# Optimization experiments

Measured on AMD Instinct MI355X. Metric: run time of the kernel, lower is better.

The kernel has to match this reference:

```python
import jax, jax.numpy as jnp
import numpy as np

B = 131072   # batch rows in the (pooled) sparse tensor
C = 512      # conv_out4
J = 7        # jnt_dim
H = 512      # linear_out
TAU_MAX = 1.0  # undefined global in source; torque cap, taken as 1.0
EPS = 1e-5


def layer_norm(x, g, b):
    m = jnp.mean(x, axis=-1, keepdims=True)
    v = jnp.var(x, axis=-1, keepdims=True)
    return (x - m) * jax.lax.rsqrt(v + EPS) * g + b


def setup_inputs() -> dict:
    key = jax.random.key(0)
    ks = jax.random.split(key, 6)
    return {
        "features": jax.random.normal(ks[0], (B, C), dtype=jnp.float32),
        "coords": jax.random.randint(ks[1], (B,), 0, B),  # batch indices (col 0 of ME coords)
        "jnt_pos": jax.random.normal(ks[2], (B, J), dtype=jnp.float32),
        "jnt_goal": jax.random.normal(ks[3], (B, J), dtype=jnp.float32),
        "ln1_g": jnp.ones((C,), jnp.float32),
        "ln1_b": jnp.zeros((C,), jnp.float32),
        "W1": jax.random.normal(ks[4], (C + 2 * J, H), dtype=jnp.float32) / np.sqrt(C + 2 * J),
        "b1": jnp.zeros((H,), jnp.float32),
        "ln2_g": jnp.ones((H,), jnp.float32),
        "ln2_b": jnp.zeros((H,), jnp.float32),
        "W2": jax.random.normal(ks[5], (H, J), dtype=jnp.float32) / np.sqrt(H),
        "b2": jnp.zeros((J,), jnp.float32),
    }


def reference(features, coords, jnt_pos, jnt_goal,
              ln1_g, ln1_b, W1, b1, ln2_g, ln2_b, W2, b2):
    # to_dense_tnsr: y = zeros_like(features); for c in coords: y[c] = features[c]
    # vectorized: single gather + scatter (duplicate writes carry identical values)
    y = jnp.zeros_like(features).at[coords].set(features[coords])
    # norm = LayerNorm(512) -> SELU   (dropout in eval mode: identity)
    x = jax.nn.selu(layer_norm(y, ln1_g, ln1_b))
    # cat((jnt_pos, jnt_goal, x), dim=1)
    x = jnp.concatenate([jnt_pos, jnt_goal, x], axis=1)  # [B, 2J+C]
    # linear = Linear -> LayerNorm -> SELU
    x = jax.nn.selu(layer_norm(x @ W1 + b1, ln2_g, ln2_b))
    # out = Linear -> Tanh, scaled by tau_max
    return jnp.tanh(x @ W2 + b2) * TAU_MAX
```

## Files before the change

### kernel.cpp

```cpp
#include <hip/hip_runtime.h>

#define B_ROWS   131072
#define MTILE    64
#define KCHUNKS  17
#define LDA      552
#define LDX      528
#define W1F_OFF  ((size_t)B_ROWS)
#define W2F_OFF  (W1F_OFF + (size_t)544 * 512 * 2)

typedef _Float16 f16x8 __attribute__((ext_vector_type(8)));
typedef float    f32x4 __attribute__((ext_vector_type(4)));

__device__ inline unsigned short f2h(float f) {
  _Float16 h = (_Float16)f;
  return __builtin_bit_cast(unsigned short, h);
}
__device__ inline float selu_f(float x) {
  const float lam = 1.0507009873554805f, alp = 1.6732632423543772f;
  return x > 0.f ? lam * x : lam * alp * (__expf(x) - 1.f);
}

__global__ void scatter_mask(const int* __restrict__ coords,
                             unsigned char* __restrict__ mask) {
  int i = blockIdx.x * 256 + threadIdx.x;
  mask[coords[i]] = 1u;
}

__global__ void build_wf(const float* __restrict__ W1, const float* __restrict__ W2,
                         unsigned short* __restrict__ W1f, unsigned short* __restrict__ W2f) {
  int tid = threadIdx.x;
  if (blockIdx.x < 544) {
    int fragIdx = blockIdx.x;
    int ni = fragIdx & 3;
    int c  = (fragIdx >> 2) % 17;
    int wq = fragIdx / 68;
    int nbase = wq * 64 + ni * 16;
    __shared__ float t[32][17];
    int kl = tid >> 4, nl = tid & 15;
    int kg = c * 32 + kl;
    float v = 0.f;
    if (kg < 512)      v = W1[(size_t)(kg + 14) * 512 + nbase + nl];
    else if (kg < 526) v = W1[(size_t)(kg - 512) * 512 + nbase + nl];
    t[kl][nl] = v;
    __syncthreads();
    int lane = tid >> 3, e = tid & 7;
    int k2 = ((lane >> 4) & 3) * 8 + e;
    int n2 = lane & 15;
    W1f[(size_t)fragIdx * 512 + tid] = f2h(t[k2][n2]);
  } else {
    int c2 = blockIdx.x - 544;
    int lane = tid >> 3, e = tid & 7;
    int n = lane & 15, quad = (lane >> 4) & 3;
    int k = c2 * 32 + quad * 8 + e;
    float v = (n < 7) ? W2[(size_t)k * 7 + n] : 0.f;
    W2f[(size_t)c2 * 512 + tid] = f2h(v);
  }
}

struct __align__(16) SMem {
  char buf[70656];
  float rsum[MTILE], rsq[MTILE], mean2[MTILE], rstd2[MTILE];
};

__global__ __launch_bounds__(512, 4) void actor_main(
    const float* __restrict__ feat, const unsigned char* __restrict__ mask,
    const float* __restrict__ jp, const float* __restrict__ jg,
    const float* __restrict__ ln1g, const float* __restrict__ ln1b,
    const unsigned short* __restrict__ W1f, const float* __restrict__ b1,
    const float* __restrict__ ln2g, const float* __restrict__ ln2b,
    const unsigned short* __restrict__ W2f, const float* __restrict__ b2,
    float* __restrict__ out) {
  __shared__ SMem sm;
  unsigned short* At = (unsigned short*)sm.buf;
  unsigned short* X2 = (unsigned short*)sm.buf;
  float*          O  = (float*)(sm.buf + 64 * LDX * 2);

  const int tid  = threadIdx.x;
  const int wq   = tid >> 6;
  const int lane = tid & 63;
  const int m0   = blockIdx.x * MTILE;
  const int mrow = lane & 15;
  const int quad = lane >> 4;

  if (tid < MTILE) { sm.rsum[tid] = 0.f; sm.rsq[tid] = 0.f; }

  const unsigned short* wBase = W1f + (size_t)wq * 68 * 512 + lane * 8;
  f16x8 bE[4], bO[4];
#pragma unroll
  for (int ni = 0; ni < 4; ++ni)
    bE[ni] = *(const f16x8*)(wBase + (size_t)ni * 512);

  {
    const int arow = tid >> 3;
    const int acg  = tid & 7;
    const int row  = m0 + arow;
    const float4* frow = (const float4*)feat + (size_t)row * 128 + acg;
    float4 f[16];
    float s = 0.f, q = 0.f;
#pragma unroll
    for (int c = 0; c < 16; ++c) {
      float4 v = frow[(size_t)c * 8];
      f[c] = v;
      s += v.x + v.y + v.z + v.w;
      q += v.x * v.x + v.y * v.y + v.z * v.z + v.w * v.w;
    }
    s += __shfl_xor(s, 1); q += __shfl_xor(q, 1);
    s += __shfl_xor(s, 2); q += __shfl_xor(q, 2);
    s += __shfl_xor(s, 4); q += __shfl_xor(q, 4);
    float mk   = mask[row] ? 1.f : 0.f;
    float mean = mk * s * (1.f / 512.f);
    float msq  = mk * q * (1.f / 512.f);
    float rstd = rsqrtf(msq - mean * mean + 1e-5f);
#pragma unroll
    for (int c = 0; c < 16; ++c) {
      float4 g = ((const float4*)ln1g)[c * 8 + acg];
      float4 b = ((const float4*)ln1b)[c * 8 + acg];
      union { unsigned short us[4]; uint2 u; } pk;
      pk.us[0] = f2h(selu_f((f[c].x * mk - mean) * rstd * g.x + b.x));
      pk.us[1] = f2h(selu_f((f[c].y * mk - mean) * rstd * g.y + b.y));
      pk.us[2] = f2h(selu_f((f[c].z * mk - mean) * rstd * g.z + b.z));
      pk.us[3] = f2h(selu_f((f[c].w * mk - mean) * rstd * g.w + b.w));
      *(uint2*)&At[arow * LDA + c * 32 + acg * 4] = pk.u;
    }
    {
      union { unsigned short us[4]; uint2 u; } pk;
#pragma unroll
      for (int q2 = 0; q2 < 4; ++q2) {
        int kk = acg * 4 + q2;
        float val = 0.f;
        if (kk < 7)       val = jp[(size_t)row * 7 + kk];
        else if (kk < 14) val = jg[(size_t)row * 7 + kk - 7];
        pk.us[q2] = f2h(val);
      }
      *(uint2*)&At[arow * LDA + 512 + acg * 4] = pk.u;
    }
  }
  __syncthreads();

  f32x4 acc[4][4];
#pragma unroll
  for (int mi = 0; mi < 4; ++mi)
#pragma unroll
    for (int ni = 0; ni < 4; ++ni) acc[mi][ni] = (f32x4){0.f, 0.f, 0.f, 0.f};

  const unsigned short* aB = At + mrow * LDA + quad * 8;

  auto loadB = [&](f16x8* dst, int c) {
#pragma unroll
    for (int ni = 0; ni < 4; ++ni)
      dst[ni] = *(const f16x8*)(wBase + (size_t)(c * 4 + ni) * 512);
  };
  auto step = [&](const f16x8* bF, int c) {
    f16x8 a[4];
#pragma unroll
    for (int mi = 0; mi < 4; ++mi)
      a[mi] = *(const f16x8*)(aB + mi * 16 * LDA + c * 32);
#pragma unroll
    for (int mi = 0; mi < 4; ++mi)
#pragma unroll
      for (int ni = 0; ni < 4; ++ni)
        acc[mi][ni] = __builtin_amdgcn_mfma_f32_16x16x32_f16(a[mi], bF[ni], acc[mi][ni], 0, 0, 0);
  };

  for (int c = 0; c < KCHUNKS - 1; c += 2) {
    loadB(bO, c + 1);
    step(bE, c);
    loadB(bE, c + 2);
    step(bO, c + 1);
  }
  step(bE, 16);

  f16x8 bW2[2];
  bW2[0] = *(const f16x8*)&W2f[(size_t)(2 * wq)     * 512 + lane * 8];
  bW2[1] = *(const f16x8*)&W2f[(size_t)(2 * wq + 1) * 512 + lane * 8];

  float b1v[4], g2v[4], bl2v[4];
#pragma unroll
  for (int ni = 0; ni < 4; ++ni) {
    int col = wq * 64 + ni * 16 + mrow;
    b1v[ni] = b1[col]; g2v[ni] = ln2g[col]; bl2v[ni] = ln2b[col];
  }
#pragma unroll
  for (int mi = 0; mi < 4; ++mi)
#pragma unroll
    for (int reg = 0; reg < 4; ++reg) {
      int r = mi * 16 + quad * 4 + reg;
      float s = 0.f, q = 0.f;
#pragma unroll
      for (int ni = 0; ni < 4; ++ni) {
        float v = acc[mi][ni][reg] + b1v[ni];
        acc[mi][ni][reg] = v;
        s += v; q += v * v;
      }
      s += __shfl_xor(s, 1); q += __shfl_xor(q, 1);
      s += __shfl_xor(s, 2); q += __shfl_xor(q, 2);
      s += __shfl_xor(s, 4); q += __shfl_xor(q, 4);
      s += __shfl_xor(s, 8); q += __shfl_xor(q, 8);
      if ((lane & 15) == 0) { atomicAdd(&sm.rsum[r], s); atomicAdd(&sm.rsq[r], q); }
    }
  __syncthreads();
  if (tid < MTILE) {
    float mean = sm.rsum[tid] * (1.f / 512.f);
    float var  = sm.rsq[tid] * (1.f / 512.f) - mean * mean;
    sm.mean2[tid] = mean;
    sm.rstd2[tid] = rsqrtf(var + 1e-5f);
  }
  O[tid] = 0.f;
  __syncthreads();
#pragma unroll
  for (int mi = 0; mi < 4; ++mi)
#pragma unroll
    for (int ni = 0; ni < 4; ++ni)
#pragma unroll
      for (int reg = 0; reg < 4; ++reg) {
        int r = mi * 16 + quad * 4 + reg;
        int col = wq * 64 + ni * 16 + mrow;
        float v = (acc[mi][ni][reg] - sm.mean2[r]) * sm.rstd2[r] * g2v[ni] + bl2v[ni];
        X2[r * LDX + col] = f2h(selu_f(v));
      }
  __syncthreads();

  {
    f32x4 acc2[4];
#pragma unroll
    for (int mi = 0; mi < 4; ++mi) acc2[mi] = (f32x4){0.f, 0.f, 0.f, 0.f};
#pragma unroll
    for (int j = 0; j < 2; ++j) {
      int c2 = 2 * wq + j;
#pragma unroll
      for (int mi = 0; mi < 4; ++mi) {
        f16x8 a = *(const f16x8*)&X2[(mi * 16 + mrow) * LDX + c2 * 32 + quad * 8];
        acc2[mi] = __builtin_amdgcn_mfma_f32_16x16x32_f16(a, bW2[j], acc2[mi], 0, 0, 0);
      }
    }
#pragma unroll
    for (int mi = 0; mi < 4; ++mi)
#pragma unroll
      for (int reg = 0; reg < 4; ++reg)
        if (mrow < 7)
          atomicAdd(&O[(mi * 16 + quad * 4 + reg) * 8 + mrow], acc2[mi][reg]);
  }
  __syncthreads();
  {
    int r = tid >> 3, c = tid & 7;
    if (c < 7)
      out[(size_t)(m0 + r) * 7 + c] = tanhf(O[tid] + b2[c]);
  }
}

extern "C" void kernel_launch(void* const* d_in, const int* in_sizes, int n_in,
                              void* d_out, int out_size, void* d_ws, size_t ws_size,
                              hipStream_t stream) {
  const float* feat  = (const float*)d_in[0];
  const int*   crd   = (const int*)d_in[1];
  const float* jp    = (const float*)d_in[2];
  const float* jg    = (const float*)d_in[3];
  const float* ln1g  = (const float*)d_in[4];
  const float* ln1b  = (const float*)d_in[5];
  const float* W1    = (const float*)d_in[6];
  const float* b1    = (const float*)d_in[7];
  const float* ln2g  = (const float*)d_in[8];
  const float* ln2b  = (const float*)d_in[9];
  const float* W2    = (const float*)d_in[10];
  const float* b2    = (const float*)d_in[11];
  float* out = (float*)d_out;

  unsigned char*  mask = (unsigned char*)d_ws;
  unsigned short* W1f  = (unsigned short*)((char*)d_ws + W1F_OFF);
  unsigned short* W2f  = (unsigned short*)((char*)d_ws + W2F_OFF);

  hipMemsetAsync(mask, 0, (size_t)B_ROWS, stream);
  scatter_mask<<<B_ROWS / 256, 256, 0, stream>>>(crd, mask);
  build_wf<<<560, 512, 0, stream>>>(W1, W2, W1f, W2f);
  actor_main<<<B_ROWS / MTILE, 512, 0, stream>>>(
      feat, mask, jp, jg, ln1g, ln1b, W1f, b1, ln2g, ln2b, W2f, b2, out);
}
```

Before: 502.1 us.

## Split LayerNorm1 into separate kernel and stream fp16 activations via global_load_lds

Moves the masking, LayerNorm1, SELU and concatenation of joint inputs into a standalone row-per-wavefront kernel that writes a padded fp16 activation matrix to workspace. The GEMM kernel then loads its A tile directly into LDS with global_load_lds and reduces LN2 statistics with shuffles plus per-wave partials instead of shared atomics. The aim is to take the LN1 prologue off the GEMM critical path and shorten its staging. In exchange it adds an extra global round-trip of about 145 MB of fp16 activations, and it falls back to the fused kernel when the workspace is too small.

```diff
diff --git a/kernel.cpp b/kernel.cpp
--- a/kernel.cpp
+++ b/kernel.cpp
@@ -7,6 +7,8 @@
 #define LDX      528
 #define W1F_OFF  ((size_t)B_ROWS)
 #define W2F_OFF  (W1F_OFF + (size_t)544 * 512 * 2)
+#define X1_OFF   (W2F_OFF + (size_t)16 * 512 * 2)
+#define X1_BYTES ((size_t)B_ROWS * LDA * 2)
 
 typedef _Float16 f16x8 __attribute__((ext_vector_type(8)));
 typedef float    f32x4 __attribute__((ext_vector_type(4)));
@@ -18,6 +20,11 @@
 __device__ inline float selu_f(float x) {
   const float lam = 1.0507009873554805f, alp = 1.6732632423543772f;
   return x > 0.f ? lam * x : lam * alp * (__expf(x) - 1.f);
+}
+__device__ inline void gld16(const void* g, void* l) {
+  __builtin_amdgcn_global_load_lds(
+      (const __attribute__((address_space(1))) unsigned int*)g,
+      (__attribute__((address_space(3))) unsigned int*)l, 16, 0, 0);
 }
 
 __global__ void scatter_mask(const int* __restrict__ coords,
@@ -57,12 +64,224 @@
   }
 }
 
-struct __align__(16) SMem {
+__global__ __launch_bounds__(512) void ln1_kernel(
+    const float* __restrict__ feat, const unsigned char* __restrict__ mask,
+    const float* __restrict__ jp, const float* __restrict__ jg,
+    const float* __restrict__ ln1g, const float* __restrict__ ln1b,
+    unsigned short* __restrict__ X1) {
+  const int w = threadIdx.x >> 6, lane = threadIdx.x & 63;
+  const size_t row = (size_t)blockIdx.x * 8 + w;
+  float mk = mask[row] ? 1.f : 0.f;
+  const float4* frow = (const float4*)feat + row * 128;
+  float4 f0 = frow[lane];
+  float4 f1 = frow[64 + lane];
+  float s = f0.x + f0.y + f0.z + f0.w + f1.x + f1.y + f1.z + f1.w;
+  float q = f0.x * f0.x + f0.y * f0.y + f0.z * f0.z + f0.w * f0.w +
+            f1.x * f1.x + f1.y * f1.y + f1.z * f1.z + f1.w * f1.w;
+#pragma unroll
+  for (int d = 32; d > 0; d >>= 1) { s += __shfl_xor(s, d); q += __shfl_xor(q, d); }
+  float mean = mk * s * (1.f / 512.f);
+  float msq  = mk * q * (1.f / 512.f);
+  float rstd = rsqrtf(msq - mean * mean + 1e-5f);
+  unsigned short* xr = X1 + row * LDA;
+  {
+    float4 g = ((const float4*)ln1g)[lane], b = ((const float4*)ln1b)[lane];
+    union { unsigned short us[4]; uint2 u; } pk;
+    pk.us[0] = f2h(selu_f((f0.x * mk - mean) * rstd * g.x + b.x));
+    pk.us[1] = f2h(selu_f((f0.y * mk - mean) * rstd * g.y + b.y));
+    pk.us[2] = f2h(selu_f((f0.z * mk - mean) * rstd * g.z + b.z));
+    pk.us[3] = f2h(selu_f((f0.w * mk - mean) * rstd * g.w + b.w));
+    *(uint2*)&xr[lane * 4] = pk.u;
+  }
+  {
+    float4 g = ((const float4*)ln1g)[64 + lane], b = ((const float4*)ln1b)[64 + lane];
+    union { unsigned short us[4]; uint2 u; } pk;
+    pk.us[0] = f2h(selu_f((f1.x * mk - mean) * rstd * g.x + b.x));
+    pk.us[1] = f2h(selu_f((f1.y * mk - mean) * rstd * g.y + b.y));
+    pk.us[2] = f2h(selu_f((f1.z * mk - mean) * rstd * g.z + b.z));
+    pk.us[3] = f2h(selu_f((f1.w * mk - mean) * rstd * g.w + b.w));
+    *(uint2*)&xr[256 + lane * 4] = pk.u;
+  }
+  if (lane < 16) {
+    int kk = 2 * lane;
+    float v0 = 0.f, v1 = 0.f;
+    if (kk < 7)       v0 = jp[row * 7 + kk];
+    else if (kk < 14) v0 = jg[row * 7 + kk - 7];
+    if (kk + 1 < 7)       v1 = jp[row * 7 + kk + 1];
+    else if (kk + 1 < 14) v1 = jg[row * 7 + kk - 6];
+    union { unsigned short us[2]; unsigned int u; } pj;
+    pj.us[0] = f2h(v0); pj.us[1] = f2h(v1);
+    *(unsigned int*)&xr[512 + 2 * lane] = pj.u;
+  } else if (lane < 20) {
+    *(unsigned int*)&xr[544 + 2 * (lane - 16)] = 0u;
+  }
+}
+
+struct __align__(16) SMemG {
+  char buf[70656];
+  float part[8][MTILE][2];
+  float mean2[MTILE], rstd2[MTILE];
+};
+
+__global__ __launch_bounds__(512, 4) void actor_gemm(
+    const unsigned short* __restrict__ X1,
+    const unsigned short* __restrict__ W1f, const float* __restrict__ b1,
+    const float* __restrict__ ln2g, const float* __restrict__ ln2b,
+    const unsigned short* __restrict__ W2f, const float* __restrict__ b2,
+    float* __restrict__ out) {
+  __shared__ SMemG sm;
+  unsigned short* At = (unsigned short*)sm.buf;
+  unsigned short* X2 = (unsigned short*)sm.buf;
+  float*          O  = (float*)(sm.buf + 64 * LDX * 2);
+
+  const int tid  = threadIdx.x;
+  const int wq   = tid >> 6;
+  const int lane = tid & 63;
+  const int m0   = blockIdx.x * MTILE;
+  const int mrow = lane & 15;
+  const int quad = lane >> 4;
+
+  {
+    const char* src = (const char*)X1 + (size_t)m0 * (LDA * 2);
+#pragma unroll
+    for (int i = 0; i < 8; ++i) {
+      int chunk = i * 8 + wq;
+      gld16(src + (size_t)chunk * 1024 + lane * 16, (char*)sm.buf + chunk * 1024);
+    }
+    if (wq < 5) {
+      int chunk = 64 + wq;
+      gld16(src + (size_t)chunk * 1024 + lane * 16, (char*)sm.buf + chunk * 1024);
+    }
+  }
+
+  const unsigned short* wBase = W1f + (size_t)wq * 68 * 512 + lane * 8;
+  f16x8 bE[4], bO[4];
+#pragma unroll
+  for (int ni = 0; ni < 4; ++ni)
+    bE[ni] = *(const f16x8*)(wBase + (size_t)ni * 512);
+
+  __syncthreads();
+
+  f32x4 acc[4][4];
+#pragma unroll
+  for (int mi = 0; mi < 4; ++mi)
+#pragma unroll
+    for (int ni = 0; ni < 4; ++ni) acc[mi][ni] = (f32x4){0.f, 0.f, 0.f, 0.f};
+
+  const unsigned short* aB = At + mrow * LDA + quad * 8;
+
+  auto loadB = [&](f16x8* dst, int c) {
+#pragma unroll
+    for (int ni = 0; ni < 4; ++ni)
+      dst[ni] = *(const f16x8*)(wBase + (size_t)(c * 4 + ni) * 512);
+  };
+  auto step = [&](const f16x8* bF, int c) {
+    f16x8 a[4];
+#pragma unroll
+    for (int mi = 0; mi < 4; ++mi)
+      a[mi] = *(const f16x8*)(aB + mi * 16 * LDA + c * 32);
+#pragma unroll
+    for (int mi = 0; mi < 4; ++mi)
+#pragma unroll
+      for (int ni = 0; ni < 4; ++ni)
+        acc[mi][ni] = __builtin_amdgcn_mfma_f32_16x16x32_f16(a[mi], bF[ni], acc[mi][ni], 0, 0, 0);
+  };
+
+  for (int c = 0; c < KCHUNKS - 1; c += 2) {
+    loadB(bO, c + 1);
+    step(bE, c);
+    loadB(bE, c + 2);
+    step(bO, c + 1);
+  }
+  step(bE, 16);
+
+  f16x8 bW2[2];
+  bW2[0] = *(const f16x8*)&W2f[(size_t)(2 * wq)     * 512 + lane * 8];
+  bW2[1] = *(const f16x8*)&W2f[(size_t)(2 * wq + 1) * 512 + lane * 8];
+
+  float b1v[4], g2v[4], bl2v[4];
+#pragma unroll
+  for (int ni = 0; ni < 4; ++ni) {
+    int col = wq * 64 + ni * 16 + mrow;
+    b1v[ni] = b1[col]; g2v[ni] = ln2g[col]; bl2v[ni] = ln2b[col];
+  }
+#pragma unroll
+  for (int mi = 0; mi < 4; ++mi)
+#pragma unroll
+    for (int reg = 0; reg < 4; ++reg) {
+      int r = mi * 16 + quad * 4 + reg;
+      float s = 0.f, q = 0.f;
+#pragma unroll
+      for (int ni = 0; ni < 4; ++ni) {
+        float v = acc[mi][ni][reg] + b1v[ni];
+        acc[mi][ni][reg] = v;
+        s += v; q += v * v;
+      }
+      s += __shfl_xor(s, 1); q += __shfl_xor(q, 1);
+      s += __shfl_xor(s, 2); q += __shfl_xor(q, 2);
+      s += __shfl_xor(s, 4); q += __shfl_xor(q, 4);
+      s += __shfl_xor(s, 8); q += __shfl_xor(q, 8);
+      if ((lane & 15) == 0) { sm.part[wq][r][0] = s; sm.part[wq][r][1] = q; }
+    }
+  __syncthreads();
+  if (tid < MTILE) {
+    float s = 0.f, q = 0.f;
+#pragma unroll
+    for (int w = 0; w < 8; ++w) { s += sm.part[w][tid][0]; q += sm.part[w][tid][1]; }
+    float mean = s * (1.f / 512.f);
+    float var  = q * (1.f / 512.f) - mean * mean;
+    sm.mean2[tid] = mean;
+    sm.rstd2[tid] = rsqrtf(var + 1e-5f);
+  }
+  O[tid] = 0.f;
+  __syncthreads();
+#pragma unroll
+  for (int mi = 0; mi < 4; ++mi)
+#pragma unroll
+    for (int ni = 0; ni < 4; ++ni)
+#pragma unroll
+      for (int reg = 0; reg < 4; ++reg) {
+        int r = mi * 16 + quad * 4 + reg;
+        int col = wq * 64 + ni * 16 + mrow;
+        float v = (acc[mi][ni][reg] - sm.mean2[r]) * sm.rstd2[r] * g2v[ni] + bl2v[ni];
+        X2[r * LDX + col] = f2h(selu_f(v));
+      }
+  __syncthreads();
+
+  {
+    f32x4 acc2[4];
+#pragma unroll
+    for (int mi = 0; mi < 4; ++mi) acc2[mi] = (f32x4){0.f, 0.f, 0.f, 0.f};
+#pragma unroll
+    for (int j = 0; j < 2; ++j) {
+      int c2 = 2 * wq + j;
+#pragma unroll
+      for (int mi = 0; mi < 4; ++mi) {
+        f16x8 a = *(const f16x8*)&X2[(mi * 16 + mrow) * LDX + c2 * 32 + quad * 8];
+        acc2[mi] = __builtin_amdgcn_mfma_f32_16x16x32_f16(a, bW2[j], acc2[mi], 0, 0, 0);
+      }
+    }
+#pragma unroll
+    for (int mi = 0; mi < 4; ++mi)
+#pragma unroll
+      for (int reg = 0; reg < 4; ++reg)
+        if (mrow < 7)
+          atomicAdd(&O[(mi * 16 + quad * 4 + reg) * 8 + mrow], acc2[mi][reg]);
+  }
+  __syncthreads();
+  {
+    int r = tid >> 3, c = tid & 7;
+    if (c < 7)
+      out[(size_t)(m0 + r) * 7 + c] = tanhf(O[tid] + b2[c]);
+  }
+}
+
+struct __align__(16) SMemF {
   char buf[70656];
   float rsum[MTILE], rsq[MTILE], mean2[MTILE], rstd2[MTILE];
 };
 
-__global__ __launch_bounds__(512, 4) void actor_main(
+__global__ __launch_bounds__(512, 4) void actor_fused(
     const float* __restrict__ feat, const unsigned char* __restrict__ mask,
     const float* __restrict__ jp, const float* __restrict__ jg,
     const float* __restrict__ ln1g, const float* __restrict__ ln1b,
@@ -70,7 +289,7 @@
     const float* __restrict__ ln2g, const float* __restrict__ ln2b,
     const unsigned short* __restrict__ W2f, const float* __restrict__ b2,
     float* __restrict__ out) {
-  __shared__ SMem sm;
+  __shared__ SMemF sm;
   unsigned short* At = (unsigned short*)sm.buf;
   unsigned short* X2 = (unsigned short*)sm.buf;
   float*          O  = (float*)(sm.buf + 64 * LDX * 2);
@@ -144,7 +363,6 @@
     for (int ni = 0; ni < 4; ++ni) acc[mi][ni] = (f32x4){0.f, 0.f, 0.f, 0.f};
 
   const unsigned short* aB = At + mrow * LDA + quad * 8;
-
   auto loadB = [&](f16x8* dst, int c) {
 #pragma unroll
     for (int ni = 0; ni < 4; ++ni)
@@ -161,7 +379,6 @@
       for (int ni = 0; ni < 4; ++ni)
         acc[mi][ni] = __builtin_amdgcn_mfma_f32_16x16x32_f16(a[mi], bF[ni], acc[mi][ni], 0, 0, 0);
   };
-
   for (int c = 0; c < KCHUNKS - 1; c += 2) {
     loadB(bO, c + 1);
     step(bE, c);
@@ -219,7 +436,6 @@
         X2[r * LDX + col] = f2h(selu_f(v));
       }
   __syncthreads();
-
   {
     f32x4 acc2[4];
 #pragma unroll
@@ -268,10 +484,18 @@
   unsigned char*  mask = (unsigned char*)d_ws;
   unsigned short* W1f  = (unsigned short*)((char*)d_ws + W1F_OFF);
   unsigned short* W2f  = (unsigned short*)((char*)d_ws + W2F_OFF);
+  unsigned short* X1   = (unsigned short*)((char*)d_ws + X1_OFF);
 
   hipMemsetAsync(mask, 0, (size_t)B_ROWS, stream);
   scatter_mask<<<B_ROWS / 256, 256, 0, stream>>>(crd, mask);
   build_wf<<<560, 512, 0, stream>>>(W1, W2, W1f, W2f);
-  actor_main<<<B_ROWS / MTILE, 512, 0, stream>>>(
-      feat, mask, jp, jg, ln1g, ln1b, W1f, b1, ln2g, ln2b, W2f, b2, out);
-}
+
+  if (ws_size >= X1_OFF + X1_BYTES) {
+    ln1_kernel<<<B_ROWS / 8, 512, 0, stream>>>(feat, mask, jp, jg, ln1g, ln1b, X1);
+    actor_gemm<<<B_ROWS / MTILE, 512, 0, stream>>>(
+        X1, W1f, b1, ln2g, ln2b, W2f, b2, out);
+  } else {
+    actor_fused<<<B_ROWS / MTILE, 512, 0, stream>>>(
+        feat, mask, jp, jg, ln1g, ln1b, W1f, b1, ln2g, ln2b, W2f, b2, out);
+  }
+}
```

After: 550.9 us. 9.7% more time.
